# Performance work log

Measured on AMD Instinct MI355X. Metric: run time of the kernel, lower is better.

Reference implementation:

```python
import jax, jax.numpy as jnp
import numpy as np

B, N, E, H, T, FC = 16, 4096, 131072, 16, 3, 20


def setup_inputs() -> dict:
    key = jax.random.key(0)
    ks = jax.random.split(key, 16)
    F = jnp.eye(3, dtype=jnp.float32)[None] + 0.05 * jax.random.normal(ks[0], (B, 3, 3), dtype=jnp.float32)
    node_pos = jax.random.uniform(ks[1], (N, 3), dtype=jnp.float32)
    edge_src = jax.random.randint(ks[2], (E,), 0, N)
    edge_dst = jax.random.randint(ks[3], (E,), 0, N)
    edge_type = jax.random.randint(ks[4], (E,), 0, T)
    sc = lambda k, s: jax.random.normal(k, s, dtype=jnp.float32) / np.float32(np.sqrt(s[0]))
    return {
        'F': F, 'node_pos': node_pos,
        'edge_src': edge_src, 'edge_dst': edge_dst, 'edge_type': edge_type,
        'W_in': sc(ks[5], (3, H)),
        'fc1_0': sc(ks[6], (T, FC)), 'fc2_0': sc(ks[7], (FC, 1)), 'W_0': sc(ks[8], (H, H)),
        'fc1_1': sc(ks[9], (T, FC)), 'fc2_1': sc(ks[10], (FC, 1)), 'W_1': sc(ks[11], (H, H)),
        'W_out': sc(ks[12], (H, 3)),
        'w': jax.random.uniform(ks[13], (N * N,), dtype=jnp.float32),
    }


def _message_passing(Fx, edge_src, edge_dst, edge_oh,
                     W_in, fc1_0, fc2_0, W_0, fc1_1, fc2_1, W_1, W_out):
    # simplified stand-in for e3nn MessagePassing_v1: per-edge scalar gate from
    # edge-type MLP (fc_neurons=[3,20]), gather-scatter aggregation / sqrt(deg)
    inv_sqrt_deg = np.float32(1.0 / np.sqrt(edge_src.shape[0] / Fx.shape[1]))
    h = Fx @ W_in  # [B,N,H]
    for fc1, fc2, Wl in ((fc1_0, fc2_0, W_0), (fc1_1, fc2_1, W_1)):
        ew = jax.nn.relu(edge_oh @ fc1) @ fc2          # [E,1]
        msg = h[:, edge_src] * ew[None]                # [B,E,H]
        agg = jnp.zeros_like(h).at[:, edge_dst].add(msg) * inv_sqrt_deg
        h = jax.nn.relu(agg @ Wl)
    return h @ W_out  # [B,N,3]


def reference(F, node_pos, edge_src, edge_dst, edge_type,
              W_in, fc1_0, fc2_0, W_0, fc1_1, fc2_1, W_1, W_out, w):
    edge_oh = jax.nn.one_hot(edge_type, T, dtype=F.dtype)
    Fx = jnp.einsum('bij,nj->bni', F, node_pos)                     # deform positions
    h = _message_passing(Fx, edge_src, edge_dst, edge_oh,
                         W_in, fc1_0, fc2_0, W_0, fc1_1, fc2_1, W_1, W_out)
    Fx_ij = h[:, edge_src] - h[:, edge_dst]                         # [B,E,3]
    x_ij = jnp.einsum('bij,bej->bei', jnp.linalg.inv(F), Fx_ij)     # [B,E,3]
    n = node_pos.shape[0]
    a = Fx_ij[:, :n]  # original loop indexes first N edges with node index i
    c = x_ij[:, :n]
    W2 = w.reshape(n, n)
    # vectorized form of: sum_ij w[i*n+j] * kron(Fx_ij[b,i], x_ij[b,j])
    t = jnp.einsum('ij,bip->bjp', W2, a)                            # [B,N,3]
    stress = jnp.einsum('bjp,bjq->bpq', t, c).reshape(F.shape[0], 9)
    return stress
```

## Files before the change

kernel.cpp:

```cpp
#include <hip/hip_runtime.h>

#define N_NODES 4096
#define N_EDGES 131072
#define BATCH   16
#define HDIM    16
#define FCDIM   20
#define BH      256
#define ISD     0.17677669529663687f
#define NBSTRESS 2048

__device__ __forceinline__ float f4get(const float4& v, int k) {
    return k == 0 ? v.x : (k == 1 ? v.y : (k == 2 ? v.z : v.w));
}

template<int CTRL, int RM>
__device__ __forceinline__ float dpp_add(float v) {
    int sh = __builtin_amdgcn_update_dpp(0, __float_as_int(v), CTRL, RM, 0xF, true);
    return v + __int_as_float(sh);
}
__device__ __forceinline__ float wave_sum64(float v) {
    v = dpp_add<0xB1, 0xF>(v);
    v = dpp_add<0x4E, 0xF>(v);
    v = dpp_add<0x141,0xF>(v);
    v = dpp_add<0x140,0xF>(v);
    v = dpp_add<0x142,0xA>(v);
    v = dpp_add<0x143,0xC>(v);
    return v;
}

__global__ void setup_kernel(const float* __restrict__ F, const float* __restrict__ W_in,
                             const float* __restrict__ fc1_0, const float* __restrict__ fc2_0,
                             const float* __restrict__ fc1_1, const float* __restrict__ fc2_1,
                             float* __restrict__ ew, float* __restrict__ G,
                             float* __restrict__ invF, float* __restrict__ out144,
                             int* __restrict__ cnt) {
    int t = threadIdx.x;
    if (t < 6) {
        const float* fc1 = (t < 3) ? fc1_0 : fc1_1;
        const float* fc2 = (t < 3) ? fc2_0 : fc2_1;
        int ty = t % 3;
        float s = 0.f;
        for (int f = 0; f < FCDIM; ++f) {
            float v = fc1[ty * FCDIM + f];
            v = v > 0.f ? v : 0.f;
            s += v * fc2[f];
        }
        ew[t] = s;
    }
    for (int idx = t; idx < BATCH * 3 * HDIM; idx += 256) {
        int b = idx / 48, r = idx % 48, j = r / HDIM, k = r % HDIM;
        float s = 0.f;
        for (int i = 0; i < 3; ++i) s += F[b * 9 + i * 3 + j] * W_in[i * HDIM + k];
        G[idx] = s;
    }
    if (t < BATCH) {
        const float* f = F + t * 9;
        float a00=f[0],a01=f[1],a02=f[2],a10=f[3],a11=f[4],a12=f[5],a20=f[6],a21=f[7],a22=f[8];
        float det = a00*(a11*a22-a12*a21) - a01*(a10*a22-a12*a20) + a02*(a10*a21-a11*a20);
        float id = 1.f/det;
        float* o = invF + t*9;
        o[0]=(a11*a22-a12*a21)*id; o[1]=(a02*a21-a01*a22)*id; o[2]=(a01*a12-a02*a11)*id;
        o[3]=(a12*a20-a10*a22)*id; o[4]=(a00*a22-a02*a20)*id; o[5]=(a02*a10-a00*a12)*id;
        o[6]=(a10*a21-a11*a20)*id; o[7]=(a01*a20-a00*a21)*id; o[8]=(a00*a11-a01*a10)*id;
    }
    if (t < 144) out144[t] = 0.f;
    for (int i = t; i < N_NODES; i += 256) cnt[i] = 0;
}

__global__ void h0_hist_kernel(const float* __restrict__ pos, const float* __restrict__ G,
                               float* __restrict__ h0,
                               const int* __restrict__ edst, int* __restrict__ cnt) {
    int bid = blockIdx.x;
    int t = threadIdx.x;
    if (bid < 1024) {
        int id = bid * 256 + t;
        int n  = id >> 6;
        int c4 = (id & 63) << 2;
        int b  = c4 >> 4;
        int k  = c4 & 15;
        float p0 = pos[n*3+0], p1 = pos[n*3+1], p2 = pos[n*3+2];
        const float* g = G + b*48 + k;
        float4 r;
        r.x = p0*g[0] + p1*g[16] + p2*g[32];
        r.y = p0*g[1] + p1*g[17] + p2*g[33];
        r.z = p0*g[2] + p1*g[18] + p2*g[34];
        r.w = p0*g[3] + p1*g[19] + p2*g[35];
        *(float4*)(h0 + n*BH + c4) = r;
    } else {
        int e = (bid - 1024) * 256 + t;
        if (e < N_EDGES) atomicAdd(&cnt[edst[e]], 1);
    }
}

__global__ void scan_kernel(const int* __restrict__ cnt, int* __restrict__ off,
                            int* __restrict__ cursor) {
    __shared__ int wsum[4];
    int t = threadIdx.x;
    int lane = t & 63, wave = t >> 6;
    int base = t * 16;
    int loc[16];
    int s = 0;
    #pragma unroll
    for (int i = 0; i < 16; ++i) { loc[i] = s; s += cnt[base + i]; }
    int pre = s;
    #pragma unroll
    for (int o = 1; o < 64; o <<= 1) {
        int v = __shfl_up(pre, o);
        if (lane >= o) pre += v;
    }
    if (lane == 63) wsum[wave] = pre;
    __syncthreads();
    int woff = 0;
    #pragma unroll
    for (int w = 0; w < 4; ++w) if (w < wave) woff += wsum[w];
    int excl = woff + pre - s;
    #pragma unroll
    for (int i = 0; i < 16; ++i) {
        int v = excl + loc[i];
        off[base + i] = v;
        cursor[base + i] = v;
    }
    if (t == 255) off[N_NODES] = excl + s;
}
__global__ void fill_kernel(const int* __restrict__ src, const int* __restrict__ dst,
                            const int* __restrict__ typ, int* __restrict__ cursor,
                            int* __restrict__ sedge) {
    int e = blockIdx.x * 256 + threadIdx.x;
    if (e < N_EDGES) {
        int p = atomicAdd(&cursor[dst[e]], 1);
        sedge[p] = src[e] | (typ[e] << 16);
    }
}

__global__ void layer_kernel(const float* __restrict__ h_in, float* __restrict__ h_out,
                             const int* __restrict__ off, const int* __restrict__ sedge,
                             const float* __restrict__ ew3, const float* __restrict__ W) {
    __shared__ float Wl[256];
    __shared__ float aggS[2][16*17 + 4];
    int t = threadIdx.x;
    Wl[t] = W[t];
    int wave = t >> 6, lane = t & 63;
    int node = wave >> 1;
    int half = wave & 1;
    int d = blockIdx.x * 2 + node;
    float e0 = ew3[0], e1 = ew3[1], e2 = ew3[2];
    int beg = off[d], end = off[d+1];
    int col = half * 128 + lane * 2;
    float2 acc = {0.f, 0.f};
    int it = beg;
    for (; it + 7 < end; it += 8) {
        int v[8]; float2 hv[8];
        #pragma unroll
        for (int u = 0; u < 8; ++u) v[u] = sedge[it + u];
        #pragma unroll
        for (int u = 0; u < 8; ++u)
            hv[u] = *(const float2*)(h_in + (v[u] & 0xFFFF) * BH + col);
        #pragma unroll
        for (int u = 0; u < 8; ++u) {
            int ty = v[u] >> 16;
            float wg = (ty == 0) ? e0 : (ty == 1 ? e1 : e2);
            acc.x += wg * hv[u].x; acc.y += wg * hv[u].y;
        }
    }
    for (; it < end; ++it) {
        int v = sedge[it];
        int ty = v >> 16;
        float wg = (ty == 0) ? e0 : (ty == 1 ? e1 : e2);
        float2 hv = *(const float2*)(h_in + (v & 0xFFFF) * BH + col);
        acc.x += wg * hv.x; acc.y += wg * hv.y;
    }
    int b = col >> 4, k0 = col & 15;
    aggS[node][b*17 + k0]     = acc.x * ISD;
    aggS[node][b*17 + k0 + 1] = acc.y * ISD;
    __syncthreads();
    int en = t >> 7, c2 = (t & 127) * 2;
    int eb = c2 >> 4, ek = c2 & 15;
    const float* arow = aggS[en] + eb * 17;
    float o0 = 0.f, o1 = 0.f;
    #pragma unroll
    for (int k = 0; k < 16; ++k) {
        float av = arow[k];
        o0 += av * Wl[k*16 + ek];
        o1 += av * Wl[k*16 + ek + 1];
    }
    int ed = blockIdx.x * 2 + en;
    float2 r;
    r.x = o0 > 0.f ? o0 : 0.f;
    r.y = o1 > 0.f ? o1 : 0.f;
    *(float2*)(h_out + ed*BH + c2) = r;
}

__global__ void ac_kernel(const float* __restrict__ h2, const float* __restrict__ Wout,
                          const int* __restrict__ esrc, const int* __restrict__ edst,
                          const float* __restrict__ invF,
                          float* __restrict__ a, float* __restrict__ c) {
    __shared__ float iF[144];
    __shared__ float Wo[48];
    int t = threadIdx.x;
    if (t < 144) iF[t] = invF[t];
    else if (t < 192) Wo[t - 144] = Wout[t - 144];
    __syncthreads();
    int id = blockIdx.x * 256 + t;
    int i = id >> 4, b = id & 15;
    int s = esrc[i], d = edst[i];
    const float* hs = h2 + s*BH + b*HDIM;
    const float* hd = h2 + d*BH + b*HDIM;
    float a0 = 0.f, a1 = 0.f, a2 = 0.f;
    #pragma unroll
    for (int k = 0; k < 16; ++k) {
        float dv = hs[k] - hd[k];
        a0 += dv*Wo[k*3+0]; a1 += dv*Wo[k*3+1]; a2 += dv*Wo[k*3+2];
    }
    float* ap = a + i*48 + b*3;
    ap[0]=a0; ap[1]=a1; ap[2]=a2;
    const float* m = iF + b*9;
    float* cp = c + i*48 + b*3;
    cp[0] = m[0]*a0 + m[1]*a1 + m[2]*a2;
    cp[1] = m[3]*a0 + m[4]*a1 + m[5]*a2;
    cp[2] = m[6]*a0 + m[7]*a1 + m[8]*a2;
}

__global__ __launch_bounds__(256, 8)
void stress_fused_kernel(const float* __restrict__ W2, const float* __restrict__ a,
                         const float* __restrict__ c, float* __restrict__ P) {
    __shared__ float sa[64 * 48];
    int t = threadIdx.x;
    int lane = t & 63;
    int wave = t >> 6;
    int cg   = wave * 12;
    int jb    = (blockIdx.x & 31) * 128;
    int strip = blockIdx.x >> 5;
    int i0    = strip * 64;
    {
        const float4* ga = (const float4*)(a + (size_t)i0 * 48);
        float4* la = (float4*)sa;
        #pragma unroll
        for (int k = 0; k < 3; ++k) la[t + k * 256] = ga[t + k * 256];
    }
    __syncthreads();
    int j = jb + lane * 2;
    const float* w2p = W2 + (size_t)i0 * N_NODES + j;
    float4 acc[2][3];
    #pragma unroll
    for (int jj = 0; jj < 2; ++jj)
        #pragma unroll
        for (int q = 0; q < 3; ++q) acc[jj][q] = make_float4(0.f,0.f,0.f,0.f);
    float2 w[8];
    #pragma unroll
    for (int u = 0; u < 8; ++u)
        w[u] = *(const float2*)(w2p + (size_t)u * N_NODES);
    #pragma unroll 1
    for (int base = 0; base < 64; base += 8) {
        float2 wn[8];
        #pragma unroll
        for (int u = 0; u < 8; ++u) {
            int r = base + 8 + u; if (r > 63) r = 63;
            wn[u] = *(const float2*)(w2p + (size_t)r * N_NODES);
        }
        #pragma unroll
        for (int u = 0; u < 8; ++u) {
            const float* ar = &sa[(base + u) * 48 + cg];
            float4 x = *(const float4*)(ar);
            float4 y = *(const float4*)(ar + 4);
            float4 z = *(const float4*)(ar + 8);
            #pragma unroll
            for (int jj = 0; jj < 2; ++jj) {
                float wv = jj == 0 ? w[u].x : w[u].y;
                acc[jj][0].x += wv*x.x; acc[jj][0].y += wv*x.y;
                acc[jj][0].z += wv*x.z; acc[jj][0].w += wv*x.w;
                acc[jj][1].x += wv*y.x; acc[jj][1].y += wv*y.y;
                acc[jj][1].z += wv*y.z; acc[jj][1].w += wv*y.w;
                acc[jj][2].x += wv*z.x; acc[jj][2].y += wv*z.y;
                acc[jj][2].z += wv*z.z; acc[jj][2].w += wv*z.w;
            }
        }
        #pragma unroll
        for (int u = 0; u < 8; ++u) w[u] = wn[u];
    }
    float s[36];
    #pragma unroll
    for (int m = 0; m < 36; ++m) s[m] = 0.f;
    #pragma unroll
    for (int jj = 0; jj < 2; ++jj) {
        const float* cvp = c + (size_t)(jb + lane * 2 + jj) * 48 + cg;
        float4 c0 = *(const float4*)(cvp);
        float4 c1 = *(const float4*)(cvp + 4);
        float4 c2 = *(const float4*)(cvp + 8);
        float cv[12] = {c0.x,c0.y,c0.z,c0.w, c1.x,c1.y,c1.z,c1.w, c2.x,c2.y,c2.z,c2.w};
        #pragma unroll
        for (int cc = 0; cc < 12; ++cc) {
            float tv = f4get(acc[jj][cc >> 2], cc & 3);
            int qb = (cc / 3) * 3;
            s[cc*3+0] += tv * cv[qb+0];
            s[cc*3+1] += tv * cv[qb+1];
            s[cc*3+2] += tv * cv[qb+2];
        }
    }
    #pragma unroll
    for (int m = 0; m < 36; ++m) s[m] = wave_sum64(s[m]);
    if (lane == 63) {
        #pragma unroll
        for (int m = 0; m < 36; ++m) {
            int cc = m / 3, q = m % 3;
            int bp = cg + cc;
            P[(size_t)((bp / 3) * 9 + (bp % 3) * 3 + q) * NBSTRESS + blockIdx.x] = s[m];
        }
    }
}

__global__ void stress_reduce_kernel(const float* __restrict__ P, float* __restrict__ out) {
    __shared__ float wsum[4];
    int t = threadIdx.x, lane = t & 63, wave = t >> 6;
    const float* p = P + (size_t)blockIdx.x * NBSTRESS;
    float4 v0 = *(const float4*)(p + t * 8);
    float4 v1 = *(const float4*)(p + t * 8 + 4);
    float s = v0.x+v0.y+v0.z+v0.w + v1.x+v1.y+v1.z+v1.w;
    #pragma unroll
    for (int o = 1; o < 64; o <<= 1) s += __shfl_xor(s, o);
    if (lane == 0) wsum[wave] = s;
    __syncthreads();
    if (t == 0) out[blockIdx.x] = wsum[0] + wsum[1] + wsum[2] + wsum[3];
}

extern "C" void kernel_launch(void* const* d_in, const int* in_sizes, int n_in,
                              void* d_out, int out_size, void* d_ws, size_t ws_size,
                              hipStream_t stream) {
    const float* F     = (const float*)d_in[0];
    const float* pos   = (const float*)d_in[1];
    const int*   esrc  = (const int*)d_in[2];
    const int*   edst  = (const int*)d_in[3];
    const int*   etyp  = (const int*)d_in[4];
    const float* W_in  = (const float*)d_in[5];
    const float* fc1_0 = (const float*)d_in[6];
    const float* fc2_0 = (const float*)d_in[7];
    const float* W_0   = (const float*)d_in[8];
    const float* fc1_1 = (const float*)d_in[9];
    const float* fc2_1 = (const float*)d_in[10];
    const float* W_1   = (const float*)d_in[11];
    const float* W_out = (const float*)d_in[12];
    const float* w2    = (const float*)d_in[13];
    float* out = (float*)d_out;

    float* ws   = (float*)d_ws;
    float* ew   = ws;
    float* G    = ws + 16;
    float* invF = ws + 800;
    float* bufA = ws + 1024;
    float* bufB = bufA + N_NODES*BH;
    float* aArr = bufB + N_NODES*BH;
    float* cArr = aArr + N_NODES*48;
    int* cnt    = (int*)(cArr + N_NODES*48);
    int* off    = cnt + N_NODES;
    int* cursor = off + N_NODES + 1;
    int* sedge  = cursor + N_NODES;
    float* P    = (float*)(sedge + N_EDGES);

    setup_kernel<<<1, 256, 0, stream>>>(F, W_in, fc1_0, fc2_0, fc1_1, fc2_1, ew, G, invF, out, cnt);
    h0_hist_kernel<<<1536, 256, 0, stream>>>(pos, G, bufA, edst, cnt);
    scan_kernel<<<1, 256, 0, stream>>>(cnt, off, cursor);
    fill_kernel<<<512, 256, 0, stream>>>(esrc, edst, etyp, cursor, sedge);
    layer_kernel<<<2048, 256, 0, stream>>>(bufA, bufB, off, sedge, ew,     W_0);
    layer_kernel<<<2048, 256, 0, stream>>>(bufB, bufA, off, sedge, ew + 3, W_1);
    ac_kernel<<<256, 256, 0, stream>>>(bufA, W_out, esrc, edst, invF, aArr, cArr);
    stress_fused_kernel<<<NBSTRESS, 256, 0, stream>>>(w2, aArr, cArr, P);
    stress_reduce_kernel<<<144, 256, 0, stream>>>(P, out);
}
```

Before: 226.0 us.

## Double stress kernel row strip to 128 and halve partial-sum blocks

The stress kernel now processes 128 rows of W2 per block instead of 64, so the grid shrinks from 2048 to 1024 blocks and the partial-reduction buffer and reduce kernel halve. The aim is to cut the per-block overhead of the cross-lane reduction and partial stores, and to fetch the c vectors once per larger tile. The W2 prefetch becomes a two-stage ping-pong of 8-row groups, and occupancy is pinned to 4 waves per EU to allow more registers. The trade-offs are double the shared memory per block, fewer blocks in flight, and more register pressure from the extra prefetch buffers. The launch configuration is not visible, so whether the grid size was changed to match cannot be confirmed.

```diff
diff --git a/kernel.cpp b/kernel.cpp
--- a/kernel.cpp
+++ b/kernel.cpp
@@ -7,7 +7,7 @@
 #define FCDIM   20
 #define BH      256
 #define ISD     0.17677669529663687f
-#define NBSTRESS 2048
+#define NBSTRESS 1024
 
 __device__ __forceinline__ float f4get(const float4& v, int k) {
     return k == 0 ? v.x : (k == 1 ? v.y : (k == 2 ? v.z : v.w));
@@ -220,22 +220,23 @@
     cp[2] = m[6]*a0 + m[7]*a1 + m[8]*a2;
 }
 
-__global__ __launch_bounds__(256, 8)
+__global__ __launch_bounds__(256)
+__attribute__((amdgpu_waves_per_eu(4, 4)))
 void stress_fused_kernel(const float* __restrict__ W2, const float* __restrict__ a,
                          const float* __restrict__ c, float* __restrict__ P) {
-    __shared__ float sa[64 * 48];
+    __shared__ float sa[128 * 48];
     int t = threadIdx.x;
     int lane = t & 63;
     int wave = t >> 6;
     int cg   = wave * 12;
     int jb    = (blockIdx.x & 31) * 128;
     int strip = blockIdx.x >> 5;
-    int i0    = strip * 64;
+    int i0    = strip * 128;
     {
         const float4* ga = (const float4*)(a + (size_t)i0 * 48);
         float4* la = (float4*)sa;
         #pragma unroll
-        for (int k = 0; k < 3; ++k) la[t + k * 256] = ga[t + k * 256];
+        for (int k = 0; k < 6; ++k) la[t + k * 256] = ga[t + k * 256];
     }
     __syncthreads();
     int j = jb + lane * 2;
@@ -245,17 +246,20 @@
     for (int jj = 0; jj < 2; ++jj)
         #pragma unroll
         for (int q = 0; q < 3; ++q) acc[jj][q] = make_float4(0.f,0.f,0.f,0.f);
-    float2 w[8];
+    float2 w0[8], w1[8];
     #pragma unroll
     for (int u = 0; u < 8; ++u)
-        w[u] = *(const float2*)(w2p + (size_t)u * N_NODES);
+        w0[u] = *(const float2*)(w2p + (size_t)u * N_NODES);
+    #pragma unroll
+    for (int u = 0; u < 8; ++u)
+        w1[u] = *(const float2*)(w2p + (size_t)(8 + u) * N_NODES);
     #pragma unroll 1
-    for (int base = 0; base < 64; base += 8) {
-        float2 wn[8];
-        #pragma unroll
-        for (int u = 0; u < 8; ++u) {
-            int r = base + 8 + u; if (r > 63) r = 63;
-            wn[u] = *(const float2*)(w2p + (size_t)r * N_NODES);
+    for (int base = 0; base < 128; base += 16) {
+        float2 n0[8], n1[8];
+        #pragma unroll
+        for (int u = 0; u < 8; ++u) {
+            int r = base + 16 + u; if (r > 127) r = 127;
+            n0[u] = *(const float2*)(w2p + (size_t)r * N_NODES);
         }
         #pragma unroll
         for (int u = 0; u < 8; ++u) {
@@ -265,7 +269,7 @@
             float4 z = *(const float4*)(ar + 8);
             #pragma unroll
             for (int jj = 0; jj < 2; ++jj) {
-                float wv = jj == 0 ? w[u].x : w[u].y;
+                float wv = jj == 0 ? w0[u].x : w0[u].y;
                 acc[jj][0].x += wv*x.x; acc[jj][0].y += wv*x.y;
                 acc[jj][0].z += wv*x.z; acc[jj][0].w += wv*x.w;
                 acc[jj][1].x += wv*y.x; acc[jj][1].y += wv*y.y;
@@ -275,7 +279,29 @@
             }
         }
         #pragma unroll
-        for (int u = 0; u < 8; ++u) w[u] = wn[u];
+        for (int u = 0; u < 8; ++u) {
+            int r = base + 24 + u; if (r > 127) r = 127;
+            n1[u] = *(const float2*)(w2p + (size_t)r * N_NODES);
+        }
+        #pragma unroll
+        for (int u = 0; u < 8; ++u) {
+            const float* ar = &sa[(base + 8 + u) * 48 + cg];
+            float4 x = *(const float4*)(ar);
+            float4 y = *(const float4*)(ar + 4);
+            float4 z = *(const float4*)(ar + 8);
+            #pragma unroll
+            for (int jj = 0; jj < 2; ++jj) {
+                float wv = jj == 0 ? w1[u].x : w1[u].y;
+                acc[jj][0].x += wv*x.x; acc[jj][0].y += wv*x.y;
+                acc[jj][0].z += wv*x.z; acc[jj][0].w += wv*x.w;
+                acc[jj][1].x += wv*y.x; acc[jj][1].y += wv*y.y;
+                acc[jj][1].z += wv*y.z; acc[jj][1].w += wv*y.w;
+                acc[jj][2].x += wv*z.x; acc[jj][2].y += wv*z.y;
+                acc[jj][2].z += wv*z.z; acc[jj][2].w += wv*z.w;
+            }
+        }
+        #pragma unroll
+        for (int u = 0; u < 8; ++u) { w0[u] = n0[u]; w1[u] = n1[u]; }
     }
     float s[36];
     #pragma unroll
@@ -312,9 +338,8 @@
     __shared__ float wsum[4];
     int t = threadIdx.x, lane = t & 63, wave = t >> 6;
     const float* p = P + (size_t)blockIdx.x * NBSTRESS;
-    float4 v0 = *(const float4*)(p + t * 8);
-    float4 v1 = *(const float4*)(p + t * 8 + 4);
-    float s = v0.x+v0.y+v0.z+v0.w + v1.x+v1.y+v1.z+v1.w;
+    float4 v = *(const float4*)(p + t * 4);
+    float s = v.x + v.y + v.z + v.w;
     #pragma unroll
     for (int o = 1; o < 64; o <<= 1) s += __shfl_xor(s, o);
     if (lane == 0) wsum[wave] = s;
```

Result: slower. 244.8 us (+8.3%).

## Replace CSR scan/fill with fixed-capacity per-node edge buckets

Applied to the files above, without the earlier changes.

Edges are bucketed directly into per-destination slots of fixed capacity (96) using an atomic counter. This removes the separate scan and fill kernels, and the G precompute moves into the h0 kernel. The layer kernel reads each node's edges from its bucket using the count. The change saves two launches and one pass over the edges, but it silently breaks if any node's in-degree exceeds the cap, and it uses a larger sedge buffer. Launch bounds on the stress kernel also drop from 8 to 6 waves.

```diff
diff --git a/kernel.cpp b/kernel.cpp
--- a/kernel.cpp
+++ b/kernel.cpp
@@ -8,6 +8,7 @@
 #define BH      256
 #define ISD     0.17677669529663687f
 #define NBSTRESS 2048
+#define DEGCAP  96
 
 __device__ __forceinline__ float f4get(const float4& v, int k) {
     return k == 0 ? v.x : (k == 1 ? v.y : (k == 2 ? v.z : v.w));
@@ -28,12 +29,11 @@
     return v;
 }
 
-__global__ void setup_kernel(const float* __restrict__ F, const float* __restrict__ W_in,
-                             const float* __restrict__ fc1_0, const float* __restrict__ fc2_0,
+__global__ void setup_kernel(const float* __restrict__ F, const float* __restrict__ fc1_0,
+                             const float* __restrict__ fc2_0,
                              const float* __restrict__ fc1_1, const float* __restrict__ fc2_1,
-                             float* __restrict__ ew, float* __restrict__ G,
-                             float* __restrict__ invF, float* __restrict__ out144,
-                             int* __restrict__ cnt) {
+                             float* __restrict__ ew, float* __restrict__ invF,
+                             float* __restrict__ out144, int* __restrict__ cnt) {
     int t = threadIdx.x;
     if (t < 6) {
         const float* fc1 = (t < 3) ? fc1_0 : fc1_1;
@@ -47,12 +47,6 @@
         }
         ew[t] = s;
     }
-    for (int idx = t; idx < BATCH * 3 * HDIM; idx += 256) {
-        int b = idx / 48, r = idx % 48, j = r / HDIM, k = r % HDIM;
-        float s = 0.f;
-        for (int i = 0; i < 3; ++i) s += F[b * 9 + i * 3 + j] * W_in[i * HDIM + k];
-        G[idx] = s;
-    }
     if (t < BATCH) {
         const float* f = F + t * 9;
         float a00=f[0],a01=f[1],a02=f[2],a10=f[3],a11=f[4],a12=f[5],a20=f[6],a21=f[7],a22=f[8];
@@ -67,9 +61,11 @@
     for (int i = t; i < N_NODES; i += 256) cnt[i] = 0;
 }
 
-__global__ void h0_hist_kernel(const float* __restrict__ pos, const float* __restrict__ G,
-                               float* __restrict__ h0,
-                               const int* __restrict__ edst, int* __restrict__ cnt) {
+__global__ void h0_fill_kernel(const float* __restrict__ pos, const float* __restrict__ F,
+                               const float* __restrict__ W_in, float* __restrict__ h0,
+                               const int* __restrict__ esrc, const int* __restrict__ edst,
+                               const int* __restrict__ etyp,
+                               int* __restrict__ cnt, int* __restrict__ sedge) {
     int bid = blockIdx.x;
     int t = threadIdx.x;
     if (bid < 1024) {
@@ -79,61 +75,31 @@
         int b  = c4 >> 4;
         int k  = c4 & 15;
         float p0 = pos[n*3+0], p1 = pos[n*3+1], p2 = pos[n*3+2];
-        const float* g = G + b*48 + k;
+        const float* f = F + b * 9;
+        float q0 = f[0]*p0 + f[1]*p1 + f[2]*p2;
+        float q1 = f[3]*p0 + f[4]*p1 + f[5]*p2;
+        float q2 = f[6]*p0 + f[7]*p1 + f[8]*p2;
+        const float* w0 = W_in + k;
+        const float* w1 = W_in + 16 + k;
+        const float* w2 = W_in + 32 + k;
         float4 r;
-        r.x = p0*g[0] + p1*g[16] + p2*g[32];
-        r.y = p0*g[1] + p1*g[17] + p2*g[33];
-        r.z = p0*g[2] + p1*g[18] + p2*g[34];
-        r.w = p0*g[3] + p1*g[19] + p2*g[35];
+        r.x = q0*w0[0] + q1*w1[0] + q2*w2[0];
+        r.y = q0*w0[1] + q1*w1[1] + q2*w2[1];
+        r.z = q0*w0[2] + q1*w1[2] + q2*w2[2];
+        r.w = q0*w0[3] + q1*w1[3] + q2*w2[3];
         *(float4*)(h0 + n*BH + c4) = r;
     } else {
         int e = (bid - 1024) * 256 + t;
-        if (e < N_EDGES) atomicAdd(&cnt[edst[e]], 1);
-    }
-}
-
-__global__ void scan_kernel(const int* __restrict__ cnt, int* __restrict__ off,
-                            int* __restrict__ cursor) {
-    __shared__ int wsum[4];
-    int t = threadIdx.x;
-    int lane = t & 63, wave = t >> 6;
-    int base = t * 16;
-    int loc[16];
-    int s = 0;
-    #pragma unroll
-    for (int i = 0; i < 16; ++i) { loc[i] = s; s += cnt[base + i]; }
-    int pre = s;
-    #pragma unroll
-    for (int o = 1; o < 64; o <<= 1) {
-        int v = __shfl_up(pre, o);
-        if (lane >= o) pre += v;
-    }
-    if (lane == 63) wsum[wave] = pre;
-    __syncthreads();
-    int woff = 0;
-    #pragma unroll
-    for (int w = 0; w < 4; ++w) if (w < wave) woff += wsum[w];
-    int excl = woff + pre - s;
-    #pragma unroll
-    for (int i = 0; i < 16; ++i) {
-        int v = excl + loc[i];
-        off[base + i] = v;
-        cursor[base + i] = v;
-    }
-    if (t == 255) off[N_NODES] = excl + s;
-}
-__global__ void fill_kernel(const int* __restrict__ src, const int* __restrict__ dst,
-                            const int* __restrict__ typ, int* __restrict__ cursor,
-                            int* __restrict__ sedge) {
-    int e = blockIdx.x * 256 + threadIdx.x;
-    if (e < N_EDGES) {
-        int p = atomicAdd(&cursor[dst[e]], 1);
-        sedge[p] = src[e] | (typ[e] << 16);
+        if (e < N_EDGES) {
+            int d = edst[e];
+            int slot = atomicAdd(&cnt[d], 1);
+            sedge[d * DEGCAP + slot] = esrc[e] | (etyp[e] << 16);
+        }
     }
 }
 
 __global__ void layer_kernel(const float* __restrict__ h_in, float* __restrict__ h_out,
-                             const int* __restrict__ off, const int* __restrict__ sedge,
+                             const int* __restrict__ cnt, const int* __restrict__ sedge,
                              const float* __restrict__ ew3, const float* __restrict__ W) {
     __shared__ float Wl[256];
     __shared__ float aggS[2][16*17 + 4];
@@ -144,7 +110,7 @@
     int half = wave & 1;
     int d = blockIdx.x * 2 + node;
     float e0 = ew3[0], e1 = ew3[1], e2 = ew3[2];
-    int beg = off[d], end = off[d+1];
+    int beg = d * DEGCAP, end = beg + cnt[d];
     int col = half * 128 + lane * 2;
     float2 acc = {0.f, 0.f};
     int it = beg;
@@ -220,7 +186,7 @@
     cp[2] = m[6]*a0 + m[7]*a1 + m[8]*a2;
 }
 
-__global__ __launch_bounds__(256, 8)
+__global__ __launch_bounds__(256, 6)
 void stress_fused_kernel(const float* __restrict__ W2, const float* __restrict__ a,
                          const float* __restrict__ c, float* __restrict__ P) {
     __shared__ float sa[64 * 48];
@@ -343,24 +309,19 @@
 
     float* ws   = (float*)d_ws;
     float* ew   = ws;
-    float* G    = ws + 16;
-    float* invF = ws + 800;
-    float* bufA = ws + 1024;
+    float* invF = ws + 16;
+    float* bufA = ws + 256;
     float* bufB = bufA + N_NODES*BH;
     float* aArr = bufB + N_NODES*BH;
     float* cArr = aArr + N_NODES*48;
     int* cnt    = (int*)(cArr + N_NODES*48);
-    int* off    = cnt + N_NODES;
-    int* cursor = off + N_NODES + 1;
-    int* sedge  = cursor + N_NODES;
-    float* P    = (float*)(sedge + N_EDGES);
-
-    setup_kernel<<<1, 256, 0, stream>>>(F, W_in, fc1_0, fc2_0, fc1_1, fc2_1, ew, G, invF, out, cnt);
-    h0_hist_kernel<<<1536, 256, 0, stream>>>(pos, G, bufA, edst, cnt);
-    scan_kernel<<<1, 256, 0, stream>>>(cnt, off, cursor);
-    fill_kernel<<<512, 256, 0, stream>>>(esrc, edst, etyp, cursor, sedge);
-    layer_kernel<<<2048, 256, 0, stream>>>(bufA, bufB, off, sedge, ew,     W_0);
-    layer_kernel<<<2048, 256, 0, stream>>>(bufB, bufA, off, sedge, ew + 3, W_1);
+    int* sedge  = cnt + N_NODES;
+    float* P    = (float*)(sedge + N_NODES*DEGCAP);
+
+    setup_kernel<<<1, 256, 0, stream>>>(F, fc1_0, fc2_0, fc1_1, fc2_1, ew, invF, out, cnt);
+    h0_fill_kernel<<<1536, 256, 0, stream>>>(pos, F, W_in, bufA, esrc, edst, etyp, cnt, sedge);
+    layer_kernel<<<2048, 256, 0, stream>>>(bufA, bufB, cnt, sedge, ew,     W_0);
+    layer_kernel<<<2048, 256, 0, stream>>>(bufB, bufA, cnt, sedge, ew + 3, W_1);
     ac_kernel<<<256, 256, 0, stream>>>(bufA, W_out, esrc, edst, invF, aArr, cArr);
     stress_fused_kernel<<<NBSTRESS, 256, 0, stream>>>(w2, aArr, cArr, P);
     stress_reduce_kernel<<<144, 256, 0, stream>>>(P, out);
```

After: 197.1 us, median of 2. 1.15x faster.
